# Kernel tuning notes

Measured on AMD Instinct MI355X. Metric: run time of the kernel, lower is better.

The kernel has to match this reference:

```python
import jax, jax.numpy as jnp
import numpy as np

N_NODES = 100000
N_EDGES = 312500
D_IN = 256
D_HID = 256
D_OUT = 1


def setup_inputs() -> dict:
    key = jax.random.key(0)
    k_z, k_e, k_w1, k_b1, k_w2, k_b2 = jax.random.split(key, 6)
    z = jax.random.normal(k_z, (N_NODES, D_IN), dtype=jnp.float32)
    edge = jax.random.randint(k_e, (2, N_EDGES), 0, N_NODES, dtype=jnp.int64)
    # PyTorch Linear: y = x @ W.T + b; store W as [out, in]
    lim1 = 1.0 / np.sqrt(D_IN)
    W1 = jax.random.uniform(k_w1, (D_HID, D_IN), jnp.float32, -lim1, lim1)
    b1 = jax.random.uniform(k_b1, (D_HID,), jnp.float32, -lim1, lim1)
    lim2 = 1.0 / np.sqrt(D_HID)
    W2 = jax.random.uniform(k_w2, (D_OUT, D_HID), jnp.float32, -lim2, lim2)
    b2 = jax.random.uniform(k_b2, (D_OUT,), jnp.float32, -lim2, lim2)
    return {"z": z, "edge": edge, "W1": W1, "b1": b1, "W2": W2, "b2": b2}


def reference(z, edge, W1, b1, W2, b2):
    # gather endpoint embeddings and multiply elementwise: [E, D_IN]
    x = z[edge[0]] * z[edge[1]]
    # dropout is identity in eval mode
    x = jnp.einsum('ed,hd->eh', x, W1) + b1  # [E, D_HID]
    x = jax.nn.elu(x)
    x = jnp.einsum('eh,oh->eo', x, W2) + b2  # [E, 1]
    return x
```

## Files before the change

### kernel.cpp

```cpp
#include <hip/hip_runtime.h>
#include <hip/hip_bf16.h>

#define N_EDGES 312500
#define N_NODES 100000
#define D 256
#define BM 256
#define TILES (BM / 32)

typedef __attribute__((ext_vector_type(8)))  short bf16x8;
typedef __attribute__((ext_vector_type(16))) float f32x16;

static __device__ __forceinline__ unsigned short f2bf(float f) {
    union { float f; unsigned u; } c; c.f = f;
    unsigned r = c.u + 0x7fffu + ((c.u >> 16) & 1u);
    return (unsigned short)(r >> 16);
}

__global__ void prep_w1(const float* __restrict__ W1, unsigned short* __restrict__ packed) {
    int t = blockIdx.x * blockDim.x + threadIdx.x;
    if (t >= 8192) return;
    int lane = t & 63;
    int ktnt = t >> 6;
    int kt = ktnt & 15;
    int nt = ktnt >> 4;
    int r  = nt * 32 + (lane & 31);
    int c0 = kt * 16 + (lane >> 5) * 8;
    const float* src = W1 + r * D + c0;
    unsigned short v[8];
#pragma unroll
    for (int j = 0; j < 8; ++j) v[j] = f2bf(src[j]);
    uint4 u;
    u.x = (unsigned)v[0] | ((unsigned)v[1] << 16);
    u.y = (unsigned)v[2] | ((unsigned)v[3] << 16);
    u.z = (unsigned)v[4] | ((unsigned)v[5] << 16);
    u.w = (unsigned)v[6] | ((unsigned)v[7] << 16);
    reinterpret_cast<uint4*>(packed)[t] = u;
}

__global__ void prep_z(const float* __restrict__ z, unsigned short* __restrict__ zb) {
    int t = blockIdx.x * blockDim.x + threadIdx.x;
    if (t >= (N_NODES * D) / 8) return;
    const float4* src = reinterpret_cast<const float4*>(z) + 2 * (size_t)t;
    float4 v0 = src[0], v1 = src[1];
    uint4 u;
    u.x = (unsigned)f2bf(v0.x) | ((unsigned)f2bf(v0.y) << 16);
    u.y = (unsigned)f2bf(v0.z) | ((unsigned)f2bf(v0.w) << 16);
    u.z = (unsigned)f2bf(v1.x) | ((unsigned)f2bf(v1.y) << 16);
    u.w = (unsigned)f2bf(v1.z) | ((unsigned)f2bf(v1.w) << 16);
    reinterpret_cast<uint4*>(zb)[t] = u;
}

template<bool ZB>
__global__ __launch_bounds__(512, 4) void edge_decoder(
    const float* __restrict__ z,
    const unsigned short* __restrict__ zb,
    const int* __restrict__ edge,
    const unsigned short* __restrict__ w1p,
    const float* __restrict__ b1,
    const float* __restrict__ W2,
    const float* __restrict__ b2,
    float* __restrict__ out)
{
    __shared__ unsigned char ldsT[2][16 * 64 * 16];
    __shared__ float  sbufp[TILES][8][32];
    __shared__ float2 epi[8][2][16];

    const int tid  = threadIdx.x;
    const int lane = tid & 63;
    const int w    = tid >> 6;
    const int blockBase = blockIdx.x * BM;

    const int gkt  = lane >> 2;
    const int gkh  = (lane >> 1) & 1;
    const int ghal = lane & 1;
    const int d0   = 4 * lane;
    const int gktx = gkt & 7;

    auto stage = [&](int t, int b) {
        unsigned char* tb = ldsT[b] + (gkt << 10);
        int tileBase = blockBase + t * 32;
#pragma unroll
        for (int j = 0; j < 4; ++j) {
            int m  = w * 4 + j;
            int e  = tileBase + m;
            int ec = e < N_EDGES ? e : (N_EDGES - 1);
            int i0 = edge[ec];
            int i1 = edge[N_EDGES + ec];
            unsigned u0, u1;
            if (ZB) {
                uint2 P = *reinterpret_cast<const uint2*>(zb + (size_t)i0 * D + d0);
                uint2 Q = *reinterpret_cast<const uint2*>(zb + (size_t)i1 * D + d0);
                __hip_bfloat162 p0 = *reinterpret_cast<__hip_bfloat162*>(&P.x);
                __hip_bfloat162 p1 = *reinterpret_cast<__hip_bfloat162*>(&P.y);
                __hip_bfloat162 q0 = *reinterpret_cast<__hip_bfloat162*>(&Q.x);
                __hip_bfloat162 q1 = *reinterpret_cast<__hip_bfloat162*>(&Q.y);
                float2 f0 = __bfloat1622float2(p0), g0 = __bfloat1622float2(q0);
                float2 f1 = __bfloat1622float2(p1), g1 = __bfloat1622float2(q1);
                __hip_bfloat162 h0 = __float22bfloat162_rn(make_float2(f0.x * g0.x, f0.y * g0.y));
                __hip_bfloat162 h1 = __float22bfloat162_rn(make_float2(f1.x * g1.x, f1.y * g1.y));
                u0 = *reinterpret_cast<unsigned*>(&h0);
                u1 = *reinterpret_cast<unsigned*>(&h1);
            } else {
                float4 p = *reinterpret_cast<const float4*>(z + (size_t)i0 * D + d0);
                float4 q = *reinterpret_cast<const float4*>(z + (size_t)i1 * D + d0);
                __hip_bfloat162 h0 = __float22bfloat162_rn(make_float2(p.x * q.x, p.y * q.y));
                __hip_bfloat162 h1 = __float22bfloat162_rn(make_float2(p.z * q.z, p.w * q.w));
                u0 = *reinterpret_cast<unsigned*>(&h0);
                u1 = *reinterpret_cast<unsigned*>(&h1);
            }
            int unit = (m + (gkh << 5)) ^ gktx;
            *reinterpret_cast<uint2*>(tb + unit * 16 + ghal * 8) = make_uint2(u0, u1);
        }
    };

    bf16x8 a[16];
    {
        const bf16x8* bp = reinterpret_cast<const bf16x8*>(w1p);
#pragma unroll
        for (int kt = 0; kt < 16; ++kt)
            a[kt] = bp[(w * 16 + kt) * 64 + lane];
    }
    if (tid < 256) {
        int w_  = tid >> 5;
        int kh_ = (tid >> 4) & 1;
        int r_  = tid & 15;
        int h   = w_ * 32 + (r_ & 3) + 8 * (r_ >> 2) + 4 * kh_;
        epi[w_][kh_][r_] = make_float2(b1[h], W2[h]);
    }
    stage(0, 0);
    __syncthreads();

    const int kh = lane >> 5;

#pragma unroll 1
    for (int t = 0; t < TILES; ++t) {
        if (t + 1 < TILES) stage(t + 1, (t + 1) & 1);

        const unsigned char* tb = ldsT[t & 1];
        f32x16 acc;
#pragma unroll
        for (int i = 0; i < 16; ++i) acc[i] = 0.f;
#pragma unroll
        for (int kt = 0; kt < 16; ++kt) {
            bf16x8 bfrag = *reinterpret_cast<const bf16x8*>(
                tb + (kt << 10) + ((lane ^ (kt & 7)) << 4));
            acc = __builtin_amdgcn_mfma_f32_32x32x16_bf16(a[kt], bfrag, acc, 0, 0, 0);
        }

        float s = 0.f;
#pragma unroll
        for (int r = 0; r < 16; ++r) {
            float2 bw = epi[w][kh][r];
            float h = acc[r] + bw.x;
            s += (h > 0.f ? h : (__expf(h) - 1.0f)) * bw.y;
        }
        s += __shfl_xor(s, 32);
        if (lane < 32) sbufp[t][w][lane] = s;

        __syncthreads();
    }

    if (tid < BM) {
        int t  = tid >> 5;
        int e  = tid & 31;
        float sum = b2[0];
#pragma unroll
        for (int ww = 0; ww < 8; ++ww) sum += sbufp[t][ww][e];
        int eo = blockBase + tid;
        if (eo < N_EDGES) out[eo] = sum;
    }
}

extern "C" void kernel_launch(void* const* d_in, const int* in_sizes, int n_in,
                              void* d_out, int out_size, void* d_ws, size_t ws_size,
                              hipStream_t stream) {
    const float* z    = (const float*)d_in[0];
    const int*   edge = (const int*)d_in[1];
    const float* W1   = (const float*)d_in[2];
    const float* b1   = (const float*)d_in[3];
    const float* W2   = (const float*)d_in[4];
    const float* b2   = (const float*)d_in[5];
    float*       out  = (float*)d_out;

    unsigned short* w1p = (unsigned short*)d_ws;
    const size_t zbOff  = 131072;
    const size_t zbNeed = zbOff + (size_t)N_NODES * D * 2;

    prep_w1<<<32, 256, 0, stream>>>(W1, w1p);

    int blocks = (N_EDGES + BM - 1) / BM;
    if (ws_size >= zbNeed) {
        unsigned short* zb = (unsigned short*)((char*)d_ws + zbOff);
        prep_z<<<(N_NODES * D / 8 + 255) / 256, 256, 0, stream>>>(z, zb);
        edge_decoder<true><<<blocks, 512, 0, stream>>>(z, zb, edge, w1p, b1, W2, b2, out);
    } else {
        edge_decoder<false><<<blocks, 512, 0, stream>>>(z, nullptr, edge, w1p, b1, W2, b2, out);
    }
}
```

Before: 103.3 us.

## Preload edge indices to LDS and split gather into issue/commit around MFMA

Edge indices for the whole block are loaded once into shared memory, so each stage no longer performs dependent global index loads. The z gathers for the next tile are issued into registers before the MFMA loop and only multiplied and written to LDS after the epilogue, so global-load latency overlaps with compute. The product is now done directly with bf16 __hmul2 instead of converting to float and back. This adds register pressure from holding P/Q across the MFMA loop, adds LDS, and changes rounding slightly.

```diff
diff --git a/kernel.cpp b/kernel.cpp
--- a/kernel.cpp
+++ b/kernel.cpp
@@ -64,6 +64,7 @@
     __shared__ unsigned char ldsT[2][16 * 64 * 16];
     __shared__ float  sbufp[TILES][8][32];
     __shared__ float2 epi[8][2][16];
+    __shared__ int    lidx[2][BM];
 
     const int tid  = threadIdx.x;
     const int lane = tid & 63;
@@ -76,49 +77,18 @@
     const int d0   = 4 * lane;
     const int gktx = gkt & 7;
 
-    auto stage = [&](int t, int b) {
-        unsigned char* tb = ldsT[b] + (gkt << 10);
-        int tileBase = blockBase + t * 32;
-#pragma unroll
-        for (int j = 0; j < 4; ++j) {
-            int m  = w * 4 + j;
-            int e  = tileBase + m;
-            int ec = e < N_EDGES ? e : (N_EDGES - 1);
-            int i0 = edge[ec];
-            int i1 = edge[N_EDGES + ec];
-            unsigned u0, u1;
-            if (ZB) {
-                uint2 P = *reinterpret_cast<const uint2*>(zb + (size_t)i0 * D + d0);
-                uint2 Q = *reinterpret_cast<const uint2*>(zb + (size_t)i1 * D + d0);
-                __hip_bfloat162 p0 = *reinterpret_cast<__hip_bfloat162*>(&P.x);
-                __hip_bfloat162 p1 = *reinterpret_cast<__hip_bfloat162*>(&P.y);
-                __hip_bfloat162 q0 = *reinterpret_cast<__hip_bfloat162*>(&Q.x);
-                __hip_bfloat162 q1 = *reinterpret_cast<__hip_bfloat162*>(&Q.y);
-                float2 f0 = __bfloat1622float2(p0), g0 = __bfloat1622float2(q0);
-                float2 f1 = __bfloat1622float2(p1), g1 = __bfloat1622float2(q1);
-                __hip_bfloat162 h0 = __float22bfloat162_rn(make_float2(f0.x * g0.x, f0.y * g0.y));
-                __hip_bfloat162 h1 = __float22bfloat162_rn(make_float2(f1.x * g1.x, f1.y * g1.y));
-                u0 = *reinterpret_cast<unsigned*>(&h0);
-                u1 = *reinterpret_cast<unsigned*>(&h1);
-            } else {
-                float4 p = *reinterpret_cast<const float4*>(z + (size_t)i0 * D + d0);
-                float4 q = *reinterpret_cast<const float4*>(z + (size_t)i1 * D + d0);
-                __hip_bfloat162 h0 = __float22bfloat162_rn(make_float2(p.x * q.x, p.y * q.y));
-                __hip_bfloat162 h1 = __float22bfloat162_rn(make_float2(p.z * q.z, p.w * q.w));
-                u0 = *reinterpret_cast<unsigned*>(&h0);
-                u1 = *reinterpret_cast<unsigned*>(&h1);
-            }
-            int unit = (m + (gkh << 5)) ^ gktx;
-            *reinterpret_cast<uint2*>(tb + unit * 16 + ghal * 8) = make_uint2(u0, u1);
-        }
-    };
-
     bf16x8 a[16];
     {
         const bf16x8* bp = reinterpret_cast<const bf16x8*>(w1p);
 #pragma unroll
         for (int kt = 0; kt < 16; ++kt)
             a[kt] = bp[(w * 16 + kt) * 64 + lane];
+    }
+    {
+        int e = blockBase + (tid & 255);
+        if (e >= N_EDGES) e = N_EDGES - 1;
+        int half = tid >> 8;
+        lidx[half][tid & 255] = edge[half * N_EDGES + e];
     }
     if (tid < 256) {
         int w_  = tid >> 5;
@@ -127,14 +97,62 @@
         int h   = w_ * 32 + (r_ & 3) + 8 * (r_ >> 2) + 4 * kh_;
         epi[w_][kh_][r_] = make_float2(b1[h], W2[h]);
     }
-    stage(0, 0);
+    __syncthreads();
+
+    uint2 P[4], Q[4];
+    auto issue = [&](int t) {
+#pragma unroll
+        for (int j = 0; j < 4; ++j) {
+            int el = t * 32 + w * 4 + j;
+            int i0 = lidx[0][el];
+            int i1 = lidx[1][el];
+            P[j] = *reinterpret_cast<const uint2*>(zb + (size_t)i0 * D + d0);
+            Q[j] = *reinterpret_cast<const uint2*>(zb + (size_t)i1 * D + d0);
+        }
+    };
+    auto commit = [&](int b) {
+        unsigned char* tb = ldsT[b] + (gkt << 10);
+#pragma unroll
+        for (int j = 0; j < 4; ++j) {
+            __hip_bfloat162 h0 = __hmul2(*reinterpret_cast<const __hip_bfloat162*>(&P[j].x),
+                                         *reinterpret_cast<const __hip_bfloat162*>(&Q[j].x));
+            __hip_bfloat162 h1 = __hmul2(*reinterpret_cast<const __hip_bfloat162*>(&P[j].y),
+                                         *reinterpret_cast<const __hip_bfloat162*>(&Q[j].y));
+            int m = w * 4 + j;
+            int unit = (m + (gkh << 5)) ^ gktx;
+            *reinterpret_cast<uint2*>(tb + unit * 16 + ghal * 8) =
+                make_uint2(*reinterpret_cast<unsigned*>(&h0),
+                           *reinterpret_cast<unsigned*>(&h1));
+        }
+    };
+    auto stage_serial = [&](int t, int b) {
+        unsigned char* tb = ldsT[b] + (gkt << 10);
+#pragma unroll
+        for (int j = 0; j < 4; ++j) {
+            int el = t * 32 + w * 4 + j;
+            int i0 = lidx[0][el];
+            int i1 = lidx[1][el];
+            float4 p = *reinterpret_cast<const float4*>(z + (size_t)i0 * D + d0);
+            float4 q = *reinterpret_cast<const float4*>(z + (size_t)i1 * D + d0);
+            __hip_bfloat162 h0 = __float22bfloat162_rn(make_float2(p.x * q.x, p.y * q.y));
+            __hip_bfloat162 h1 = __float22bfloat162_rn(make_float2(p.z * q.z, p.w * q.w));
+            int m = w * 4 + j;
+            int unit = (m + (gkh << 5)) ^ gktx;
+            *reinterpret_cast<uint2*>(tb + unit * 16 + ghal * 8) =
+                make_uint2(*reinterpret_cast<unsigned*>(&h0),
+                           *reinterpret_cast<unsigned*>(&h1));
+        }
+    };
+
+    if constexpr (ZB) { issue(0); commit(0); }
+    else              { stage_serial(0, 0); }
     __syncthreads();
 
     const int kh = lane >> 5;
 
 #pragma unroll 1
     for (int t = 0; t < TILES; ++t) {
-        if (t + 1 < TILES) stage(t + 1, (t + 1) & 1);
+        if constexpr (ZB) { if (t + 1 < TILES) issue(t + 1); }
 
         const unsigned char* tb = ldsT[t & 1];
         f32x16 acc;
@@ -156,6 +174,9 @@
         }
         s += __shfl_xor(s, 32);
         if (lane < 32) sbufp[t][w][lane] = s;
+
+        if constexpr (ZB) { if (t + 1 < TILES) commit((t + 1) & 1); }
+        else              { if (t + 1 < TILES) stage_serial(t + 1, (t + 1) & 1); }
 
         __syncthreads();
     }
```

New measurement: 96.03 us. 1.08x faster.
